# Optimization experiments

Measured on AMD Instinct MI355X. Metric: run time of the kernel, lower is better.

Reference implementation:

```python
import jax, jax.numpy as jnp
import numpy as np

N_HEADS = 8
D_MODEL = 256
HEAD_DEPTH = D_MODEL // N_HEADS
B, S = 2, 4096


def setup_inputs() -> dict:
    key = jax.random.key(0)
    ks = jax.random.split(key, 8)
    scale = 1.0 / np.sqrt(D_MODEL)
    return {
        "q": jax.random.normal(ks[0], (B, S, D_MODEL), dtype=jnp.float32),
        "k": jax.random.normal(ks[1], (B, S, D_MODEL), dtype=jnp.float32),
        "v": jax.random.normal(ks[2], (B, S, D_MODEL), dtype=jnp.float32),
        "mask": jax.random.randint(ks[3], (B, S, S), 0, 2).astype(jnp.bool_),
        "wq": jax.random.normal(ks[4], (D_MODEL, D_MODEL), dtype=jnp.float32) * scale,
        "wk": jax.random.normal(ks[5], (D_MODEL, D_MODEL), dtype=jnp.float32) * scale,
        "wv": jax.random.normal(ks[6], (D_MODEL, D_MODEL), dtype=jnp.float32) * scale,
        "w_out": jax.random.normal(ks[7], (D_MODEL, D_MODEL), dtype=jnp.float32) * scale,
    }


def _split_heads(x):
    # [B, S, D] -> [B, H, S, Dh]
    b, s, _ = x.shape
    return x.reshape(b, s, N_HEADS, HEAD_DEPTH).transpose(0, 2, 1, 3)


def reference(q, k, v, mask, wq, wk, wv, w_out):
    Q = _split_heads(q @ wq)
    K = _split_heads(k @ wk)
    V = _split_heads(v @ wv)
    # [B, H, Sq, Sk]
    scores = jnp.einsum('bhqd,bhkd->bhqk', Q, K) / jnp.sqrt(
        jnp.asarray(HEAD_DEPTH, dtype=Q.dtype))
    # mask True -> -inf, broadcast over heads
    scores = jnp.where(mask[:, None, :, :], -jnp.inf, scores)
    probs = jax.nn.softmax(scores, axis=-1)
    attn = jnp.einsum('bhqk,bhkd->bhqd', probs, V)
    attn = attn.transpose(0, 2, 1, 3).reshape(q.shape[0], -1, D_MODEL)
    return attn @ w_out
```

## Files before the change

### kernel.cpp

```cpp
#include <hip/hip_runtime.h>
#include <stdint.h>

typedef __bf16 bf16;
typedef __bf16 bf16x8 __attribute__((ext_vector_type(8)));
typedef __bf16 bf16x4 __attribute__((ext_vector_type(4)));
typedef float  f32x4  __attribute__((ext_vector_type(4)));
typedef float  f32x8  __attribute__((ext_vector_type(8)));
typedef float  f32x16 __attribute__((ext_vector_type(16)));
typedef float  float4v __attribute__((ext_vector_type(4)));
typedef int    int4v   __attribute__((ext_vector_type(4)));
typedef unsigned int uint;
typedef unsigned long long ull;

#define QSCALE 0.25505003984214403f


__global__ __launch_bounds__(256) void transpose_w(
    const float* __restrict__ w0, const float* __restrict__ w1,
    const float* __restrict__ w2, const float* __restrict__ w3,
    bf16* __restrict__ WT) {
  const int wsel = blockIdx.z;
  const float* W = wsel == 0 ? w0 : wsel == 1 ? w1 : wsel == 2 ? w2 : w3;
  const int k0 = blockIdx.x * 64, n0 = blockIdx.y * 64;
  __shared__ __align__(16) bf16 t[64][72];
  const int tid = threadIdx.x;
  {
    const int kk = (tid >> 4) << 2;
    const int nn = (tid & 15) << 2;
#pragma unroll
    for (int r = 0; r < 4; ++r) {
      float4v a = *(const float4v*)(W + (size_t)(k0 + kk + r) * 256 + n0 + nn);
#pragma unroll
      for (int j = 0; j < 4; ++j) t[nn + j][kk + r] = (bf16)a[j];
    }
  }
  __syncthreads();
  {
    const int ni = tid >> 2;
    const int c  = (tid & 3) * 16;
    bf16x8 o0 = *(const bf16x8*)(&t[ni][c]);
    bf16x8 o1 = *(const bf16x8*)(&t[ni][c + 8]);
    bf16* dst = WT + (size_t)wsel * 65536 + (size_t)(n0 + ni) * 256 + k0 + c;
    *(bf16x8*)dst = o0;
    *(bf16x8*)(dst + 8) = o1;
  }
}

__global__ __launch_bounds__(256) void proj_pack(
    const float* __restrict__ xq, const float* __restrict__ xk, const float* __restrict__ xv,
    const bf16* __restrict__ WT,
    bf16* __restrict__ Qp, bf16* __restrict__ Kp, bf16* __restrict__ Vp,
    const int* __restrict__ mask, uint* __restrict__ M2) {
  __shared__ __align__(16) unsigned char smem[18432];
  const int tid = threadIdx.x;

  if (blockIdx.x >= 768) {
    uint* lds32 = (uint*)smem;
    const int pid = blockIdx.x - 768;
    const int bb = pid >> 8;
    const int qt = (pid >> 2) & 63, kc = pid & 3;
    const int q0 = qt * 64;
    const int w = tid >> 6, l = tid & 63;
#pragma unroll 2
    for (int r = 0; r < 16; ++r) {
      const int row = w * 16 + r;
      const size_t rowbase = ((size_t)(bb * 4096 + q0 + row)) * 4096 + kc * 1024;
      uint u = 0;
#pragma unroll
      for (int i = 0; i < 4; ++i) {
        int4v m = *(const int4v*)(mask + rowbase + i * 256 + l * 4);
        uint nib = (m[0] != 0 ? 1u : 0u) | (m[1] != 0 ? 2u : 0u) |
                   (m[2] != 0 ? 4u : 0u) | (m[3] != 0 ? 8u : 0u);
        u |= nib << (i * 8);
      }
      lds32[row * 65 + l] = u;
    }
    __syncthreads();
    {
      const int q = tid & 63, kg = tid >> 6;
      const uint* lrow = lds32 + q * 65;
      const int sh = kg * 8;
      uint* o = M2 + ((size_t)(bb * 128 + kc * 32 + kg * 8)) * 4096 + q0 + q;
#pragma unroll
      for (int j = 0; j < 8; ++j) {
        uint d = 0;
#pragma unroll
        for (int jj = 0; jj < 8; ++jj) {
          const uint wv = lrow[j * 8 + jj];
          d |= ((wv >> sh) & 0xFu) << (jj * 4);
        }
        o[(size_t)j * 4096] = d;
      }
    }
    return;
  }

  const int z = blockIdx.x >> 8;
  const int r8 = blockIdx.x & 255;
  const int m0 = (r8 >> 1) * 64, n0 = (r8 & 1) * 128;
  const float* X = z == 0 ? xq : (z == 1 ? xk : xv);
  const bf16* wt = WT + (size_t)z * 65536;
  const int wave = tid >> 6, lane = tid & 63;
  const int nl = lane & 15, quad = lane >> 4;
  const int arow = m0 + wave * 16 + nl;
  const float* xrow = X + (size_t)arow * 256;

  f32x4 zero4 = {0.f, 0.f, 0.f, 0.f};
  f32x4 acc[8];
#pragma unroll
  for (int i = 0; i < 8; ++i) acc[i] = zero4;

  for (int ks = 0; ks < 8; ++ks) {
    float4v a0 = *(const float4v*)(xrow + ks * 32 + quad * 8);
    float4v a1 = *(const float4v*)(xrow + ks * 32 + quad * 8 + 4);
    bf16x8 af;
#pragma unroll
    for (int i = 0; i < 4; ++i) { af[i] = (bf16)a0[i]; af[4 + i] = (bf16)a1[i]; }
#pragma unroll
    for (int nf = 0; nf < 8; ++nf) {
      bf16x8 bfr = *(const bf16x8*)(wt + (size_t)(n0 + nf * 16 + nl) * 256 + ks * 32 + quad * 8);
      acc[nf] = __builtin_amdgcn_mfma_f32_16x16x32_bf16(af, bfr, acc[nf], 0, 0, 0);
    }
  }

  const int bq = m0 >> 12;
  const int s0 = m0 & 4095;
  const int posl = wave * 16 + quad * 4;

  if (z == 2) {
    bf16* tv = (bf16*)smem;
#pragma unroll
    for (int nf = 0; nf < 8; ++nf) {
      const int col = nf * 16 + nl;
      bf16x4 o;
#pragma unroll
      for (int rr = 0; rr < 4; ++rr) o[rr] = (bf16)acc[nf][rr];
      *(bf16x4*)(tv + (size_t)col * 72 + posl) = o;
    }
    __syncthreads();
    const int h2 = tid >> 6, ln = tid & 63;
    const int d = ln & 31, shalf = ln >> 5;
    const int h = (n0 >> 5) + h2;
    bf16* vb = Vp + (size_t)(bq * 8 + h) * 131072 + (size_t)(s0 >> 5) * 1024 + d * 8;
#pragma unroll
    for (int it = 0; it < 4; ++it) {
      const int blk = it >> 1, sub = (it & 1) * 2 + shalf;
      const int K0 = (sub >> 1) * 16 + (sub & 1) * 4;
      const bf16* src = tv + (size_t)(h2 * 32 + d) * 72 + blk * 32 + K0;
      bf16x4 g0 = *(const bf16x4*)(src);
      bf16x4 g1 = *(const bf16x4*)(src + 8);
      bf16x8 o;
#pragma unroll
      for (int j = 0; j < 4; ++j) { o[j] = g0[j]; o[4 + j] = g1[j]; }
      *(bf16x8*)(vb + (size_t)blk * 1024 + sub * 256) = o;
    }
  } else {
    bf16* tq = (bf16*)smem;
    const float scale = (z == 0) ? QSCALE : 1.0f;
#pragma unroll
    for (int nf = 0; nf < 8; ++nf) {
      const int col = nf * 16 + nl;
#pragma unroll
      for (int rr = 0; rr < 4; ++rr)
        tq[(size_t)(posl + rr) * 136 + col] = (bf16)(acc[nf][rr] * scale);
    }
    __syncthreads();
    bf16* Out = z == 0 ? Qp : Kp;
    const int h2 = tid >> 6, ln = tid & 63;
    const int h = (n0 >> 5) + h2;
    const int s = s0 + ln;
    bf16* ob = Out + (size_t)(bq * 8 + h) * 131072 + (size_t)(s >> 5) * 1024 + (s & 31) * 8;
#pragma unroll
    for (int sub = 0; sub < 4; ++sub) {
      bf16x8 o = *(const bf16x8*)(tq + (size_t)ln * 136 + h2 * 32 + sub * 8);
      *(bf16x8*)(ob + sub * 256) = o;
    }
  }
}

__global__ __launch_bounds__(256)
__attribute__((amdgpu_waves_per_eu(4, 4)))
void attn_kernel(
    const bf16* __restrict__ Qp, const bf16* __restrict__ Kp,
    const bf16* __restrict__ Vp, const uint* __restrict__ M2,
    bf16* __restrict__ Og) {
  const int id = blockIdx.x;
  const int xcd = id & 7, slot = id >> 3;
  const int bh = xcd * 2 + (slot >> 6);
  const int q0 = (slot & 63) * 64;
  const int b = bh >> 3, h = bh & 7;
  const int tid = threadIdx.x, w = tid >> 6, lane = tid & 63;
  const int nl = lane & 31, half = lane >> 5;
  const int qsub = w & 1, kh = w >> 1;

  __shared__ float Ored[4][32][33];
  __shared__ float Lsum[32][8];

  const size_t bhbase = (size_t)bh * 131072;
  const int so0 = half * 256 + nl * 8;
  const int so1 = 512 + half * 256 + nl * 8;

  bf16x8 qf0, qf1;
  {
    const bf16* qb = Qp + bhbase + (size_t)((q0 >> 5) + qsub) * 1024;
    qf0 = *(const bf16x8*)(qb + so0);
    qf1 = *(const bf16x8*)(qb + so1);
  }

  const bf16* Kw = Kp + bhbase + (size_t)kh * 65536;
  const bf16* Vw = Vp + bhbase + (size_t)kh * 65536;
  const uint* Mw = M2 + (size_t)b * 524288 + (size_t)kh * 262144 + q0 + qsub * 32 + nl;

  f32x16 acc;
#pragma unroll
  for (int i = 0; i < 16; ++i) acc[i] = 0.f;
  f32x4 ls = {0.f, 0.f, 0.f, 0.f};

  struct Frag { bf16x8 ka0, ka1, va0, va1; uint m0; };
  auto LOADF = [&](int kt) -> Frag {
    Frag f;
    const bf16* kc = Kw + (size_t)kt * 1024;
    const bf16* vc = Vw + (size_t)kt * 1024;
    f.ka0 = *(const bf16x8*)(kc + so0);
    f.ka1 = *(const bf16x8*)(kc + so1);
    f.va0 = *(const bf16x8*)(vc + so0);
    f.va1 = *(const bf16x8*)(vc + so1);
    f.m0 = Mw[(size_t)kt * 4096];
    return f;
  };

  auto STEP = [&](const Frag& f) {
    const int mpos = (int)(f.m0 >> (4 * half));
    f32x16 bias;
#pragma unroll
    for (int g = 0; g < 4; ++g)
#pragma unroll
      for (int r = 0; r < 4; ++r) {
        const int i = g * 4 + r, off = r + 8 * g;
        const uint mb = (uint)__builtin_amdgcn_sbfe(mpos, off, 1);
        bias[i] = __uint_as_float(mb & 0xFF800000u);
      }
    __builtin_amdgcn_s_setprio(1);
    f32x16 st = __builtin_amdgcn_mfma_f32_32x32x16_bf16(f.ka0, qf0, bias, 0, 0, 0);
    st = __builtin_amdgcn_mfma_f32_32x32x16_bf16(f.ka1, qf1, st, 0, 0, 0);
    __builtin_amdgcn_s_setprio(0);

    f32x16 pf;
#pragma unroll
    for (int g = 0; g < 4; ++g)
#pragma unroll
      for (int r = 0; r < 4; ++r) {
        const int i = g * 4 + r;
        const float e = __builtin_amdgcn_exp2f(st[i]);
        ls[g] += e;
        pf[i] = e;
      }

    const bf16x8 pb0 = __builtin_convertvector(
        __builtin_shufflevector(pf, pf, 0, 1, 2, 3, 4, 5, 6, 7), bf16x8);
    const bf16x8 pb1 = __builtin_convertvector(
        __builtin_shufflevector(pf, pf, 8, 9, 10, 11, 12, 13, 14, 15), bf16x8);

    __builtin_amdgcn_s_setprio(1);
    acc = __builtin_amdgcn_mfma_f32_32x32x16_bf16(f.va0, pb0, acc, 0, 0, 0);
    acc = __builtin_amdgcn_mfma_f32_32x32x16_bf16(f.va1, pb1, acc, 0, 0, 0);
    __builtin_amdgcn_s_setprio(0);
  };

  Frag fa = LOADF(0), fb;
  for (int kt = 0; kt < 64; kt += 2) {
    if (kt && !(kt & 3)) __builtin_amdgcn_s_barrier();
    fb = LOADF(kt + 1);
    STEP(fa);
    if (kt + 2 < 64) fa = LOADF(kt + 2);
    STEP(fb);
  }

#pragma unroll
  for (int g = 0; g < 4; ++g)
#pragma unroll
    for (int r = 0; r < 4; ++r) {
      const int d = r + 8 * g + 4 * half, i = g * 4 + r;
      Ored[w][d][nl] = acc[i];
    }
  Lsum[nl][w * 2 + half] = (ls[0] + ls[1]) + (ls[2] + ls[3]);
  __syncthreads();
  {
    const int q = tid >> 2, d0 = (tid & 3) * 8;
    const int qq = q & 31, qs = q >> 5;
    const float s = (Lsum[qq][qs * 2] + Lsum[qq][qs * 2 + 1]) +
                    (Lsum[qq][(qs + 2) * 2] + Lsum[qq][(qs + 2) * 2 + 1]);
    const float rl = 1.0f / s;
    bf16x8 o;
#pragma unroll
    for (int dj = 0; dj < 8; ++dj) {
      const int d = d0 + dj;
      const float sum = Ored[qs][d][qq] + Ored[qs + 2][d][qq];
      o[dj] = (bf16)(sum * rl);
    }
    *(bf16x8*)(Og + ((size_t)(b * 4096 + q0 + q)) * 256 + h * 32 + d0) = o;
  }
}

__global__ __launch_bounds__(256, 2) void gemm_out(
    const bf16* __restrict__ A, const bf16* __restrict__ WTo, float* __restrict__ C) {
  const int m0 = blockIdx.x * 64, n0 = blockIdx.y * 64;
  const int tid = threadIdx.x, wave = tid >> 6, lane = tid & 63;
  const int nl = lane & 15, quad = lane >> 4;
  const int arow = m0 + wave * 16 + nl;

  f32x4 zero4 = {0.f, 0.f, 0.f, 0.f};
  f32x4 acc[4];
#pragma unroll
  for (int i = 0; i < 4; ++i) acc[i] = zero4;

  for (int ks = 0; ks < 8; ++ks) {
    bf16x8 af = *(const bf16x8*)(A + (size_t)arow * 256 + ks * 32 + quad * 8);
#pragma unroll
    for (int nf = 0; nf < 4; ++nf) {
      bf16x8 bfr = *(const bf16x8*)(WTo + (size_t)(n0 + nf * 16 + nl) * 256 + ks * 32 + quad * 8);
      acc[nf] = __builtin_amdgcn_mfma_f32_16x16x32_bf16(af, bfr, acc[nf], 0, 0, 0);
    }
  }
  const int Rbase = m0 + wave * 16 + quad * 4;
#pragma unroll
  for (int nf = 0; nf < 4; ++nf)
#pragma unroll
    for (int r = 0; r < 4; ++r)
      C[(size_t)(Rbase + r) * 256 + n0 + nf * 16 + nl] = acc[nf][r];
}

extern "C" void kernel_launch(void* const* d_in, const int* in_sizes, int n_in,
                              void* d_out, int out_size, void* d_ws, size_t ws_size,
                              hipStream_t stream) {
  const float* q  = (const float*)d_in[0];
  const float* k  = (const float*)d_in[1];
  const float* v  = (const float*)d_in[2];
  const int*  mask = (const int*)d_in[3];
  const float* wq = (const float*)d_in[4];
  const float* wk = (const float*)d_in[5];
  const float* wv = (const float*)d_in[6];
  const float* wo = (const float*)d_in[7];
  float* out = (float*)d_out;

  uint8_t* ws = (uint8_t*)d_ws;
  bf16* WT = (bf16*)ws;
  bf16* Qp = (bf16*)(ws + (512u << 10));
  bf16* Kp = Qp + 2097152;
  bf16* Vp = Kp + 2097152;
  uint* Mb = (uint*)((uint8_t*)(Vp + 2097152));
  bf16* Ao = (bf16*)((uint8_t*)Mb + (4u << 20));

  transpose_w<<<dim3(4, 4, 4), 256, 0, stream>>>(wq, wk, wv, wo, WT);
  proj_pack<<<dim3(768 + 512), 256, 0, stream>>>(q, k, v, WT, Qp, Kp, Vp, mask, Mb);
  attn_kernel<<<dim3(1024), 256, 0, stream>>>(Qp, Kp, Vp, Mb, Ao);
  gemm_out<<<dim3(128, 4), 256, 0, stream>>>(Ao, WT + 3 * 65536, out);
}
```

Before: 310.4 us.

## Share K/V tiles across waves via LDS double-buffering with 128-query blocks

After: 330.3 us. 6.4% more time.

```diff
diff --git a/kernel.cpp b/kernel.cpp
--- a/kernel.cpp
+++ b/kernel.cpp
@@ -5,12 +5,10 @@
 typedef __bf16 bf16x8 __attribute__((ext_vector_type(8)));
 typedef __bf16 bf16x4 __attribute__((ext_vector_type(4)));
 typedef float  f32x4  __attribute__((ext_vector_type(4)));
-typedef float  f32x8  __attribute__((ext_vector_type(8)));
 typedef float  f32x16 __attribute__((ext_vector_type(16)));
 typedef float  float4v __attribute__((ext_vector_type(4)));
 typedef int    int4v   __attribute__((ext_vector_type(4)));
 typedef unsigned int uint;
-typedef unsigned long long ull;
 
 #define QSCALE 0.25505003984214403f
 
@@ -186,15 +184,15 @@
     bf16* __restrict__ Og) {
   const int id = blockIdx.x;
   const int xcd = id & 7, slot = id >> 3;
-  const int bh = xcd * 2 + (slot >> 6);
-  const int q0 = (slot & 63) * 64;
+  const int bh = xcd * 2 + (slot >> 5);
+  const int q0 = (slot & 31) * 128;
   const int b = bh >> 3, h = bh & 7;
   const int tid = threadIdx.x, w = tid >> 6, lane = tid & 63;
   const int nl = lane & 31, half = lane >> 5;
-  const int qsub = w & 1, kh = w >> 1;
-
+
+  __shared__ __align__(16) bf16 kvbuf[2][2048];
   __shared__ float Ored[4][32][33];
-  __shared__ float Lsum[32][8];
+  __shared__ float Lsum[4][2][32];
 
   const size_t bhbase = (size_t)bh * 131072;
   const int so0 = half * 256 + nl * 8;
@@ -202,35 +200,32 @@
 
   bf16x8 qf0, qf1;
   {
-    const bf16* qb = Qp + bhbase + (size_t)((q0 >> 5) + qsub) * 1024;
+    const bf16* qb = Qp + bhbase + (size_t)((q0 >> 5) + w) * 1024;
     qf0 = *(const bf16x8*)(qb + so0);
     qf1 = *(const bf16x8*)(qb + so1);
   }
 
-  const bf16* Kw = Kp + bhbase + (size_t)kh * 65536;
-  const bf16* Vw = Vp + bhbase + (size_t)kh * 65536;
-  const uint* Mw = M2 + (size_t)b * 524288 + (size_t)kh * 262144 + q0 + qsub * 32 + nl;
+  const bf16* Kb = Kp + bhbase;
+  const bf16* Vb = Vp + bhbase;
+  const bf16* segsrc = ((w & 2) ? Vb : Kb) + (w & 1) * 512 + lane * 8;
+  const uint* Mw = M2 + (size_t)b * 524288 + q0 + w * 32 + nl;
 
   f32x16 acc;
 #pragma unroll
   for (int i = 0; i < 16; ++i) acc[i] = 0.f;
   f32x4 ls = {0.f, 0.f, 0.f, 0.f};
 
-  struct Frag { bf16x8 ka0, ka1, va0, va1; uint m0; };
-  auto LOADF = [&](int kt) -> Frag {
-    Frag f;
-    const bf16* kc = Kw + (size_t)kt * 1024;
-    const bf16* vc = Vw + (size_t)kt * 1024;
-    f.ka0 = *(const bf16x8*)(kc + so0);
-    f.ka1 = *(const bf16x8*)(kc + so1);
-    f.va0 = *(const bf16x8*)(vc + so0);
-    f.va1 = *(const bf16x8*)(vc + so1);
-    f.m0 = Mw[(size_t)kt * 4096];
-    return f;
+  auto STAGE = [&](int buf, int kt) {
+    const bf16* src = segsrc + (size_t)kt * 1024;
+    bf16* dst = &kvbuf[buf][w * 512];
+    __builtin_amdgcn_global_load_lds(
+        (const __attribute__((address_space(1))) unsigned int*)src,
+        (__attribute__((address_space(3))) unsigned int*)dst, 16, 0, 0);
   };
 
-  auto STEP = [&](const Frag& f) {
-    const int mpos = (int)(f.m0 >> (4 * half));
+  auto STEP = [&](const bf16x8& ka0, const bf16x8& ka1,
+                  const bf16x8& va0, const bf16x8& va1, uint m0) {
+    const int mpos = (int)(m0 >> (4 * half));
     f32x16 bias;
 #pragma unroll
     for (int g = 0; g < 4; ++g)
@@ -241,8 +236,8 @@
         bias[i] = __uint_as_float(mb & 0xFF800000u);
       }
     __builtin_amdgcn_s_setprio(1);
-    f32x16 st = __builtin_amdgcn_mfma_f32_32x32x16_bf16(f.ka0, qf0, bias, 0, 0, 0);
-    st = __builtin_amdgcn_mfma_f32_32x32x16_bf16(f.ka1, qf1, st, 0, 0, 0);
+    f32x16 st = __builtin_amdgcn_mfma_f32_32x32x16_bf16(ka0, qf0, bias, 0, 0, 0);
+    st = __builtin_amdgcn_mfma_f32_32x32x16_bf16(ka1, qf1, st, 0, 0, 0);
     __builtin_amdgcn_s_setprio(0);
 
     f32x16 pf;
@@ -255,25 +250,32 @@
         ls[g] += e;
         pf[i] = e;
       }
-
     const bf16x8 pb0 = __builtin_convertvector(
         __builtin_shufflevector(pf, pf, 0, 1, 2, 3, 4, 5, 6, 7), bf16x8);
     const bf16x8 pb1 = __builtin_convertvector(
         __builtin_shufflevector(pf, pf, 8, 9, 10, 11, 12, 13, 14, 15), bf16x8);
 
     __builtin_amdgcn_s_setprio(1);
-    acc = __builtin_amdgcn_mfma_f32_32x32x16_bf16(f.va0, pb0, acc, 0, 0, 0);
-    acc = __builtin_amdgcn_mfma_f32_32x32x16_bf16(f.va1, pb1, acc, 0, 0, 0);
+    acc = __builtin_amdgcn_mfma_f32_32x32x16_bf16(va0, pb0, acc, 0, 0, 0);
+    acc = __builtin_amdgcn_mfma_f32_32x32x16_bf16(va1, pb1, acc, 0, 0, 0);
     __builtin_amdgcn_s_setprio(0);
   };
 
-  Frag fa = LOADF(0), fb;
-  for (int kt = 0; kt < 64; kt += 2) {
-    if (kt && !(kt & 3)) __builtin_amdgcn_s_barrier();
-    fb = LOADF(kt + 1);
-    STEP(fa);
-    if (kt + 2 < 64) fa = LOADF(kt + 2);
-    STEP(fb);
+  STAGE(0, 0);
+  uint m_cur = Mw[0];
+  __syncthreads();
+  int cur = 0;
+  for (int kt = 0; kt < 128; ++kt) {
+    if (kt + 1 < 128) STAGE(cur ^ 1, kt + 1);
+    const uint m_next = (kt + 1 < 128) ? Mw[(size_t)(kt + 1) * 4096] : 0u;
+    const bf16x8 ka0 = *(const bf16x8*)&kvbuf[cur][lane * 8];
+    const bf16x8 ka1 = *(const bf16x8*)&kvbuf[cur][512 + lane * 8];
+    const bf16x8 va0 = *(const bf16x8*)&kvbuf[cur][1024 + lane * 8];
+    const bf16x8 va1 = *(const bf16x8*)&kvbuf[cur][1536 + lane * 8];
+    STEP(ka0, ka1, va0, va1, m_cur);
+    __syncthreads();
+    cur ^= 1;
+    m_cur = m_next;
   }
 
 #pragma unroll
@@ -283,22 +285,21 @@
       const int d = r + 8 * g + 4 * half, i = g * 4 + r;
       Ored[w][d][nl] = acc[i];
     }
-  Lsum[nl][w * 2 + half] = (ls[0] + ls[1]) + (ls[2] + ls[3]);
+  Lsum[w][half][nl] = (ls[0] + ls[1]) + (ls[2] + ls[3]);
   __syncthreads();
   {
-    const int q = tid >> 2, d0 = (tid & 3) * 8;
-    const int qq = q & 31, qs = q >> 5;
-    const float s = (Lsum[qq][qs * 2] + Lsum[qq][qs * 2 + 1]) +
-                    (Lsum[qq][(qs + 2) * 2] + Lsum[qq][(qs + 2) * 2 + 1]);
-    const float rl = 1.0f / s;
-    bf16x8 o;
-#pragma unroll
-    for (int dj = 0; dj < 8; ++dj) {
-      const int d = d0 + dj;
-      const float sum = Ored[qs][d][qq] + Ored[qs + 2][d][qq];
-      o[dj] = (bf16)(sum * rl);
-    }
-    *(bf16x8*)(Og + ((size_t)(b * 4096 + q0 + q)) * 256 + h * 32 + d0) = o;
+    const int ql = tid >> 1, dh = tid & 1;
+    const int wq = ql >> 5, qq = ql & 31;
+    const float rl = 1.0f / (Lsum[wq][0][qq] + Lsum[wq][1][qq]);
+    bf16x8 o0, o1;
+#pragma unroll
+    for (int j = 0; j < 8; ++j) {
+      o0[j] = (bf16)(Ored[wq][dh * 16 + j][qq] * rl);
+      o1[j] = (bf16)(Ored[wq][dh * 16 + 8 + j][qq] * rl);
+    }
+    bf16* ob = Og + ((size_t)(b * 4096 + q0 + ql)) * 256 + h * 32 + dh * 16;
+    *(bf16x8*)ob = o0;
+    *(bf16x8*)(ob + 8) = o1;
   }
 }
 
@@ -353,6 +354,6 @@
 
   transpose_w<<<dim3(4, 4, 4), 256, 0, stream>>>(wq, wk, wv, wo, WT);
   proj_pack<<<dim3(768 + 512), 256, 0, stream>>>(q, k, v, WT, Qp, Kp, Vp, mask, Mb);
-  attn_kernel<<<dim3(1024), 256, 0, stream>>>(Qp, Kp, Vp, Mb, Ao);
+  attn_kernel<<<dim3(512), 256, 0, stream>>>(Qp, Kp, Vp, Mb, Ao);
   gemm_out<<<dim3(128, 4), 256, 0, stream>>>(Ao, WT + 3 * 65536, out);
 }
```
